# Kernel tuning notes

Measured on AMD Instinct MI355X. Metric: run time of the kernel, lower is better.

The kernel has to match this reference:

```python
import jax, jax.numpy as jnp
import numpy as np

FEAT = 0          # feature column used by the heuristic (init kwarg feat=0)
G = 500_000       # n_groups (3D points)
N = 2_000_000     # n_items (point-pixel mappings), == csr_idx[-1]
D = 128           # modality feature dim
F = 8             # number of handcrafted mapping features


def setup_inputs() -> dict:
    key = jax.random.key(0)
    k1, k2, k3, k4 = jax.random.split(key, 4)
    x_main = jax.random.normal(k1, (G, D), dtype=jnp.float32)
    x_mod = jax.random.normal(k2, (N, D), dtype=jnp.float32)
    x_map = jax.random.uniform(k3, (N, F), dtype=jnp.float32)
    # CSR pointers: sorted boundaries with endpoints 0 and N (some groups may be empty)
    inner = jnp.sort(jax.random.randint(k4, (G - 1,), 0, N + 1, dtype=jnp.int32))
    csr_idx = jnp.concatenate([jnp.zeros((1,), jnp.int32), inner,
                               jnp.full((1,), N, jnp.int32)])
    return {"x_main": x_main, "x_mod": x_mod, "x_map": x_map, "csr_idx": csr_idx}


def reference(x_main, x_mod, x_map, csr_idx):
    n_groups = csr_idx.shape[0] - 1
    n_items = x_mod.shape[0]

    # dense_idx[i] = group of item i  (equivalent to arange(G).repeat_interleave(counts))
    item_ids = jnp.arange(n_items, dtype=csr_idx.dtype)
    dense_idx = jnp.searchsorted(csr_idx[1:], item_ids, side='right')

    # Segmented argmax on the heuristic feature column (mode='max', feat=FEAT).
    vals = x_map[:, FEAT]
    gmax = jax.ops.segment_max(vals, dense_idx, num_segments=n_groups)
    # smallest item index attaining the group max; empty groups -> n_items
    cand = jnp.where(vals == gmax[dense_idx],
                     jnp.arange(n_items, dtype=jnp.int32), n_items)
    arg_idx = jnp.minimum(
        jax.ops.segment_min(cand, dense_idx, num_segments=n_groups), n_items)

    # torch_scatter convention: empty groups point to the appended zero row.
    x_mod_0 = jnp.concatenate(
        [x_mod, jnp.zeros((1, x_mod.shape[1]), x_mod.dtype)], axis=0)
    x_pool = x_mod_0[arg_idx]                 # [G, D] gather pooling
    x_seen = csr_idx[1:] > csr_idx[:-1]       # [G] bool: group has >=1 mapping
    return x_pool, x_seen
```

## Files before the change

### kernel.cpp

```cpp
#include <hip/hip_runtime.h>


#define D_DIM 128
#define F_COLS 8

__global__ void csr_argmax_kernel(const float* __restrict__ x_map,
                                  const int* __restrict__ csr_idx,
                                  int* __restrict__ arg_out,
                                  float* __restrict__ seen_out,
                                  int n_groups, int n_items) {
    int g = blockIdx.x * blockDim.x + threadIdx.x;
    if (g >= n_groups) return;
    int start = csr_idx[g];
    int end   = csr_idx[g + 1];
    float best = -INFINITY;
    int arg = n_items;
    for (int i = start; i < end; ++i) {
        float v = x_map[(size_t)i * F_COLS];
        if (v > best) { best = v; arg = i; }
    }
    arg_out[g]  = arg;
    seen_out[g] = (end > start) ? 1.0f : 0.0f;
}

__global__ void pool_gather_kernel(const float* __restrict__ x_mod,
                                   const int* __restrict__ arg_in,
                                   float* __restrict__ x_pool,
                                   int n_groups, int n_items) {
    int lane = threadIdx.x & 31;
    int g = blockIdx.x * (blockDim.x >> 5) + (threadIdx.x >> 5);
    if (g >= n_groups) return;
    int a = arg_in[g];
    float4 v = make_float4(0.f, 0.f, 0.f, 0.f);
    if (a < n_items) {
        v = ((const float4*)(x_mod + (size_t)a * D_DIM))[lane];
    }
    ((float4*)(x_pool + (size_t)g * D_DIM))[lane] = v;
}

extern "C" void kernel_launch(void* const* d_in, const int* in_sizes, int n_in,
                              void* d_out, int out_size, void* d_ws, size_t ws_size,
                              hipStream_t stream) {
    const float* x_mod   = (const float*)d_in[1];
    const float* x_map   = (const float*)d_in[2];
    const int*   csr_idx = (const int*)d_in[3];

    const int n_items  = in_sizes[1] / D_DIM;
    const int n_groups = in_sizes[3] - 1;

    float* x_pool = (float*)d_out;
    float* x_seen = (float*)d_out + (size_t)n_groups * D_DIM;

    int* arg_ws = (int*)d_ws;

    {
        const int block = 256;
        const int grid = (n_groups + block - 1) / block;
        csr_argmax_kernel<<<grid, block, 0, stream>>>(x_map, csr_idx, arg_ws,
                                                      x_seen, n_groups, n_items);
    }
    {
        const int block = 256;
        const int grid = (n_groups + 7) / 8;
        pool_gather_kernel<<<grid, block, 0, stream>>>(x_mod, arg_ws, x_pool,
                                                       n_groups, n_items);
    }
}
```

Measured before the change: 1.347 ms.

## Fuse CSR argmax and row gather into one kernel with nontemporal copies

Merges the segmented argmax and the pooled-row gather into a single kernel. Each block computes argmax indices for 256 groups into shared memory, then its eight 32-lane groups copy the selected x_mod rows with nontemporal loads and stores. This removes the second launch and the workspace round trip for the indices. In exchange, the gather phase in each block must wait for that block's slowest group scan, and the grid is much smaller than the previous gather grid, which may reduce memory-level parallelism.

New measurement: 1.342 ms. No clear change (-0.4%).

```diff
diff --git a/kernel.cpp b/kernel.cpp
--- a/kernel.cpp
+++ b/kernel.cpp
@@ -3,39 +3,54 @@
 
 #define D_DIM 128
 #define F_COLS 8
+#define GROUPS_PER_BLOCK 256
+#define BLOCK_THREADS 256
 
-__global__ void csr_argmax_kernel(const float* __restrict__ x_map,
-                                  const int* __restrict__ csr_idx,
-                                  int* __restrict__ arg_out,
-                                  float* __restrict__ seen_out,
-                                  int n_groups, int n_items) {
-    int g = blockIdx.x * blockDim.x + threadIdx.x;
-    if (g >= n_groups) return;
-    int start = csr_idx[g];
-    int end   = csr_idx[g + 1];
-    float best = -INFINITY;
-    int arg = n_items;
-    for (int i = start; i < end; ++i) {
-        float v = x_map[(size_t)i * F_COLS];
-        if (v > best) { best = v; arg = i; }
+typedef float f4 __attribute__((ext_vector_type(4)));
+
+__global__ __launch_bounds__(BLOCK_THREADS) void fused_csr_pool_kernel(
+    const float* __restrict__ x_mod,
+    const float* __restrict__ x_map,
+    const int*   __restrict__ csr_idx,
+    float* __restrict__ x_pool,
+    float* __restrict__ x_seen,
+    int n_groups, int n_items)
+{
+    __shared__ int s_arg[GROUPS_PER_BLOCK];
+
+    const int g0 = blockIdx.x * GROUPS_PER_BLOCK;
+    const int g  = g0 + threadIdx.x;
+
+    if (g < n_groups) {
+        const int start = csr_idx[g];
+        const int end   = csr_idx[g + 1];
+        float best = -INFINITY;
+        int   arg  = n_items;
+        for (int i = start; i < end; ++i) {
+            float v = x_map[(size_t)i * F_COLS];
+            if (v > best) { best = v; arg = i; }
+        }
+        s_arg[threadIdx.x] = arg;
+        x_seen[g] = (end > start) ? 1.0f : 0.0f;
     }
-    arg_out[g]  = arg;
-    seen_out[g] = (end > start) ? 1.0f : 0.0f;
-}
+    __syncthreads();
 
-__global__ void pool_gather_kernel(const float* __restrict__ x_mod,
-                                   const int* __restrict__ arg_in,
-                                   float* __restrict__ x_pool,
-                                   int n_groups, int n_items) {
-    int lane = threadIdx.x & 31;
-    int g = blockIdx.x * (blockDim.x >> 5) + (threadIdx.x >> 5);
-    if (g >= n_groups) return;
-    int a = arg_in[g];
-    float4 v = make_float4(0.f, 0.f, 0.f, 0.f);
-    if (a < n_items) {
-        v = ((const float4*)(x_mod + (size_t)a * D_DIM))[lane];
+    const int lane = threadIdx.x & 31;
+    const int warp = threadIdx.x >> 5;
+    #pragma unroll 4
+    for (int k = 0; k < GROUPS_PER_BLOCK / 8; ++k) {
+        const int gl = warp + k * 8;
+        const int gg = g0 + gl;
+        if (gg >= n_groups) continue;
+        const int a = s_arg[gl];
+        f4 v = (f4){0.f, 0.f, 0.f, 0.f};
+        if (a < n_items) {
+            const f4* src = (const f4*)(x_mod + (size_t)a * D_DIM);
+            v = __builtin_nontemporal_load(src + lane);
+        }
+        f4* dst = (f4*)(x_pool + (size_t)gg * D_DIM);
+        __builtin_nontemporal_store(v, dst + lane);
     }
-    ((float4*)(x_pool + (size_t)g * D_DIM))[lane] = v;
 }
 
 extern "C" void kernel_launch(void* const* d_in, const int* in_sizes, int n_in,
@@ -51,18 +66,7 @@
     float* x_pool = (float*)d_out;
     float* x_seen = (float*)d_out + (size_t)n_groups * D_DIM;
 
-    int* arg_ws = (int*)d_ws;
-
-    {
-        const int block = 256;
-        const int grid = (n_groups + block - 1) / block;
-        csr_argmax_kernel<<<grid, block, 0, stream>>>(x_map, csr_idx, arg_ws,
-                                                      x_seen, n_groups, n_items);
-    }
-    {
-        const int block = 256;
-        const int grid = (n_groups + 7) / 8;
-        pool_gather_kernel<<<grid, block, 0, stream>>>(x_mod, arg_ws, x_pool,
-                                                       n_groups, n_items);
-    }
+    const int grid = (n_groups + GROUPS_PER_BLOCK - 1) / GROUPS_PER_BLOCK;
+    fused_csr_pool_kernel<<<grid, BLOCK_THREADS, 0, stream>>>(
+        x_mod, x_map, csr_idx, x_pool, x_seen, n_groups, n_items);
 }
```
